# Kernel tuning notes

Hardware: AMD Instinct MI355X
Metric: run time of the kernel (lower is better)

The kernel has to match this reference:

```python
import jax, jax.numpy as jnp
import numpy as np

N_NODES = 50000
N_EDGES = 1600000
D = 64  # in_features == out_features (required by residual index_add)
N_NBR_FEA = 41


def setup_inputs() -> dict:
    key = jax.random.key(0)
    k1, k2, k3, k4, k5 = jax.random.split(key, 5)
    return {
        "x": jax.random.normal(k1, (N_NODES, D), dtype=jnp.float32),
        # torch Linear(in=D, out=2D, bias=False): weight shape [2D, D]
        "W": jax.random.normal(k2, (2 * D, D), dtype=jnp.float32) * (1.0 / np.sqrt(D)),
        "edge_sources": jax.random.randint(k3, (N_EDGES,), 0, N_NODES),
        "edge_targets": jax.random.randint(k4, (N_EDGES,), 0, N_NODES),
        # required forward arg; unused when use_distance_nbr=False
        "distance_nbr": jax.random.normal(k5, (N_EDGES, N_NBR_FEA), dtype=jnp.float32),
    }


def reference(x, W, edge_sources, edge_targets, distance_nbr):
    # gather neighbor (target) node features per edge: [E, D]
    h = x[edge_targets]
    # edge linear -> gate + message halves: [E, 2D]
    ge = h @ W.T
    g, e = jnp.split(ge, 2, axis=1)
    msg = jax.nn.sigmoid(g) * e  # gate_activation = Sigmoid(); edge/node activations are None
    # output = input.clone(); output.index_add_(0, edge_sources, g * e)
    return x.at[edge_sources].add(msg)
```

## Files before the change

### kernel.cpp

```cpp
#include <hip/hip_runtime.h>

#define NDIM 64
#define WPAD 68
#define BINSHIFT 8
#define BINSZ 256
#define LCAP 12288
#define EPT 16
#define PCHUNK (256 * EPT)
#define NMB 512
#define PB  256

typedef unsigned short ushort;

__device__ __forceinline__ ushort f2bf(float f) {
    unsigned u = __float_as_uint(f);
    return (ushort)((u + 0x7FFFu + ((u >> 16) & 1u)) >> 16);
}
__device__ __forceinline__ float bflo(unsigned u) { return __uint_as_float(u << 16); }
__device__ __forceinline__ float bfhi(unsigned u) { return __uint_as_float(u & 0xFFFF0000u); }

__device__ void node_msg_body(
    const float* __restrict__ x, const float* __restrict__ W,
    ushort* __restrict__ Mb, int n_nodes, int bid, int nblocks)
{
    __shared__ float sW[128 * WPAD];
    __shared__ float sx[4][4][64];

    for (int i = threadIdx.x; i < 128 * 64; i += 256)
        sW[(i >> 6) * WPAD + (i & 63)] = W[i];
    __syncthreads();

    const int wid  = threadIdx.x >> 6;
    const int lane = threadIdx.x & 63;
    const float4* __restrict__ wg4 = (const float4*)&sW[lane * WPAD];
    const float4* __restrict__ we4 = (const float4*)&sW[(lane + 64) * WPAD];
    const size_t half_off = (size_t)(lane >> 5) * n_nodes * 32 + (lane & 31);

    int n0 = (bid * 4 + wid) * 4;
    int stride = nblocks * 16;
    for (; n0 < n_nodes; n0 += stride) {
        #pragma unroll
        for (int q = 0; q < 4; ++q) {
            int n = n0 + q;
            sx[wid][q][lane] = (n < n_nodes) ? x[(size_t)n * NDIM + lane] : 0.0f;
        }
        float g[4] = {0, 0, 0, 0}, e[4] = {0, 0, 0, 0};
        #pragma unroll
        for (int k4 = 0; k4 < 16; ++k4) {
            float4 a = wg4[k4];
            float4 b = we4[k4];
            #pragma unroll
            for (int q = 0; q < 4; ++q) {
                float4 xk = *(const float4*)&sx[wid][q][k4 * 4];
                g[q] = fmaf(xk.x, a.x, g[q]); g[q] = fmaf(xk.y, a.y, g[q]);
                g[q] = fmaf(xk.z, a.z, g[q]); g[q] = fmaf(xk.w, a.w, g[q]);
                e[q] = fmaf(xk.x, b.x, e[q]); e[q] = fmaf(xk.y, b.y, e[q]);
                e[q] = fmaf(xk.z, b.z, e[q]); e[q] = fmaf(xk.w, b.w, e[q]);
            }
        }
        #pragma unroll
        for (int q = 0; q < 4; ++q) {
            int n = n0 + q;
            if (n < n_nodes)
                Mb[half_off + (size_t)n * 32] = f2bf(e[q] / (1.0f + __expf(-g[q])));
        }
    }
}

__device__ void partition_body(
    const int* __restrict__ src, const int* __restrict__ tgt,
    int* __restrict__ binCursor, unsigned* __restrict__ binned,
    int n_edges, int nbins, int bid, int nblocks)
{
    __shared__ int h[256];
    __shared__ int base[256];
    const int tid = threadIdx.x;

    long long cb = (long long)bid * PCHUNK;
    long long cs = (long long)nblocks * PCHUNK;
    for (; cb < n_edges; cb += cs) {
        if (tid < nbins) h[tid] = 0;
        __syncthreads();

        unsigned pk[EPT]; ushort ps[EPT]; short pb[EPT];
        #pragma unroll
        for (int r = 0; r < EPT; ++r) {
            long long e = cb + r * 256 + tid;
            pb[r] = -1;
            if (e < n_edges) {
                int s = src[e], t = tgt[e];
                int b = s >> BINSHIFT;
                pk[r] = ((unsigned)(s & (BINSZ - 1)) << 16) | (unsigned)t;
                ps[r] = (ushort)atomicAdd(&h[b], 1);
                pb[r] = (short)b;
            }
        }
        __syncthreads();
        if (tid < nbins) {
            int c = h[tid];
            base[tid] = c ? atomicAdd(&binCursor[tid], c) : 0;
        }
        __syncthreads();
        #pragma unroll
        for (int r = 0; r < EPT; ++r) {
            if (pb[r] >= 0) {
                unsigned d = (unsigned)base[pb[r]] + ps[r];
                if (d < LCAP) binned[(size_t)pb[r] * LCAP + d] = pk[r];
            }
        }
        __syncthreads();
    }
}

__global__ __launch_bounds__(256) void fused_msg_partition_kernel(
    const float* __restrict__ x, const float* __restrict__ W,
    ushort* __restrict__ Mb, const int* __restrict__ src,
    const int* __restrict__ tgt, int* __restrict__ binCursor,
    unsigned* __restrict__ binned, int n_nodes, int n_edges, int nbins)
{
    if (blockIdx.x < NMB)
        node_msg_body(x, W, Mb, n_nodes, blockIdx.x, NMB);
    else
        partition_body(src, tgt, binCursor, binned, n_edges, nbins,
                       blockIdx.x - NMB, PB);
}

__global__ __launch_bounds__(512) void csr_build_kernel(
    const unsigned* __restrict__ binned, const int* __restrict__ binCursor,
    unsigned* __restrict__ node_meta, ushort* __restrict__ entries, int n_nodes)
{
    __shared__ unsigned sE[LCAP];
    __shared__ ushort   sT[LCAP];
    __shared__ int sCnt[BINSZ];
    __shared__ int sOff[BINSZ + 1];
    __shared__ int sCur[BINSZ];

    const int bin = blockIdx.x;
    const int tid = threadIdx.x;
    const int cnt = min(binCursor[bin], LCAP);
    const unsigned* __restrict__ be = &binned[(size_t)bin * LCAP];

    for (int i = tid; i < cnt; i += 512) sE[i] = be[i];
    for (int i = tid; i < BINSZ; i += 512) sCnt[i] = 0;
    for (int i = tid; i < LCAP / 2; i += 512) ((unsigned*)sT)[i] = 0;
    __syncthreads();

    for (int i = tid; i < cnt; i += 512) atomicAdd(&sCnt[sE[i] >> 16], 1);
    __syncthreads();

    if (tid < 64) {
        int c[4]; int s = 0;
        #pragma unroll
        for (int q = 0; q < 4; ++q) { c[q] = (sCnt[tid * 4 + q] + 7) & ~7; s += c[q]; }
        int incl = s;
        #pragma unroll
        for (int d = 1; d < 64; d <<= 1) {
            int t = __shfl_up(incl, d);
            if (tid >= d) incl += t;
        }
        int excl = incl - s;
        #pragma unroll
        for (int q = 0; q < 4; ++q) { sOff[tid * 4 + q] = excl; excl += c[q]; }
        if (tid == 63) sOff[BINSZ] = excl;
    }
    __syncthreads();
    if (tid < BINSZ) sCur[tid] = sOff[tid];
    __syncthreads();

    for (int i = tid; i < cnt; i += 512) {
        unsigned p = sE[i];
        int pos = atomicAdd(&sCur[p >> 16], 1);
        sT[pos] = (ushort)(p & 0xFFFFu);
    }

    const int gbase = bin * LCAP;
    if (tid < BINSZ) {
        int n = (bin << BINSHIFT) + tid;
        if (n < n_nodes)
            node_meta[n] = ((unsigned)(gbase + sOff[tid]) << 8)
                         | (unsigned)min(sCnt[tid], 255);
    }
    __syncthreads();

    const int tot = sOff[BINSZ];
    uint4* __restrict__ dstv = (uint4*)&entries[gbase];
    const uint4* __restrict__ srcv = (const uint4*)sT;
    for (int i = tid; i < tot / 8; i += 512) dstv[i] = srcv[i];
}

__global__ __launch_bounds__(256) void gather_half_kernel(
    const float* __restrict__ x, const ushort* __restrict__ Mbh,
    const unsigned* __restrict__ node_meta, const ushort* __restrict__ entries,
    float* __restrict__ out, int n_nodes, int half)
{
    const int wid  = threadIdx.x >> 6;
    const int lane = threadIdx.x & 63;
    const int sub  = lane >> 2;
    const int sl   = lane & 3;

    int n = (blockIdx.x * 4 + wid) * 16 + sub;
    bool valid = n < n_nodes;
    int nn = valid ? n : 0;
    unsigned meta = valid ? node_meta[nn] : 0u;
    int cnt = (int)(meta & 255u);
    const ushort* __restrict__ brow = &entries[meta >> 8];

    float acc[8] = {0, 0, 0, 0, 0, 0, 0, 0};
    for (int j = 0; j < cnt; j += 8) {
        uint4 nb = *(const uint4*)&brow[j];
        unsigned id[8] = { nb.x & 0xFFFFu, nb.x >> 16, nb.y & 0xFFFFu, nb.y >> 16,
                           nb.z & 0xFFFFu, nb.z >> 16, nb.w & 0xFFFFu, nb.w >> 16 };
        #pragma unroll
        for (int k = 0; k < 8; ++k) {
            if (j + k < cnt) {
                uint4 v = *(const uint4*)&Mbh[(size_t)id[k] * 32 + sl * 8];
                acc[0] += bflo(v.x); acc[1] += bfhi(v.x);
                acc[2] += bflo(v.y); acc[3] += bfhi(v.y);
                acc[4] += bflo(v.z); acc[5] += bfhi(v.z);
                acc[6] += bflo(v.w); acc[7] += bfhi(v.w);
            }
        }
    }
    if (valid) {
        size_t base = (size_t)n * NDIM + half * 32 + sl * 8;
        float4 x0 = *(const float4*)&x[base];
        float4 x1 = *(const float4*)&x[base + 4];
        float4 o0 = {x0.x + acc[0], x0.y + acc[1], x0.z + acc[2], x0.w + acc[3]};
        float4 o1 = {x1.x + acc[4], x1.y + acc[5], x1.z + acc[6], x1.w + acc[7]};
        *(float4*)&out[base]     = o0;
        *(float4*)&out[base + 4] = o1;
    }
}

__global__ __launch_bounds__(256) void copy_out_kernel(
    const float* __restrict__ x, float* __restrict__ out, size_t n)
{
    size_t i = (size_t)blockIdx.x * 256 + threadIdx.x;
    size_t gs = (size_t)gridDim.x * 256;
    for (; i < n; i += gs) out[i] = x[i];
}

__global__ __launch_bounds__(256) void edge_scatter_kernel(
    const int* __restrict__ src, const int* __restrict__ tgt,
    const ushort* __restrict__ Mb, float* __restrict__ out,
    int n_edges, int n_nodes)
{
    long long total = (long long)n_edges * 16;
    long long i0 = (long long)blockIdx.x * blockDim.x + threadIdx.x;
    long long gs = (long long)gridDim.x * blockDim.x;
    for (long long i = i0; i < total; i += gs) {
        int e = (int)(i >> 4);
        int q = (int)(i & 15);
        int s = src[e];
        int t = tgt[e];
        int half = q >> 2;
        int d    = (q * 4) & 31;
        uint2 v = *(const uint2*)&Mb[(size_t)half * n_nodes * 32
                                     + (size_t)t * 32 + d];
        float* o = &out[(size_t)s * NDIM + q * 4];
        atomicAdd(o + 0, bflo(v.x));
        atomicAdd(o + 1, bfhi(v.x));
        atomicAdd(o + 2, bflo(v.y));
        atomicAdd(o + 3, bfhi(v.y));
    }
}

static inline size_t align16(size_t v) { return (v + 15) & ~(size_t)15; }

extern "C" void kernel_launch(void* const* d_in, const int* in_sizes, int n_in,
                              void* d_out, int out_size, void* d_ws, size_t ws_size,
                              hipStream_t stream)
{
    const float* x   = (const float*)d_in[0];
    const float* W   = (const float*)d_in[1];
    const int*   src = (const int*)d_in[2];
    const int*   tgt = (const int*)d_in[3];

    int n_nodes = in_sizes[0] / NDIM;
    int n_edges = in_sizes[2];
    float* out = (float*)d_out;

    int nbins = (n_nodes + BINSZ - 1) >> BINSHIFT;

    char* ws = (char*)d_ws;
    size_t off = 0;
    ushort* Mb = (ushort*)(ws + off);            off = align16(off + (size_t)n_nodes * NDIM * 2);
    unsigned* node_meta = (unsigned*)(ws + off); off = align16(off + (size_t)n_nodes * 4);
    int* binCursor = (int*)(ws + off);           off = align16(off + (size_t)nbins * 4);
    unsigned* binned = (unsigned*)(ws + off);    off = align16(off + (size_t)nbins * LCAP * 4);
    ushort* entries = (ushort*)(ws + off);       off = align16(off + (size_t)nbins * LCAP * 2);
    size_t need = off + 1024;

    if (ws_size >= need && n_nodes <= 65536 && nbins <= 256) {
        hipMemsetAsync(binCursor, 0, (size_t)nbins * sizeof(int), stream);
        fused_msg_partition_kernel<<<NMB + PB, 256, 0, stream>>>(
            x, W, Mb, src, tgt, binCursor, binned, n_nodes, n_edges, nbins);
        csr_build_kernel<<<nbins, 512, 0, stream>>>(
            binned, binCursor, node_meta, entries, n_nodes);
        int gb = (n_nodes + 63) / 64;
        gather_half_kernel<<<gb, 256, 0, stream>>>(
            x, Mb, node_meta, entries, out, n_nodes, 0);
        gather_half_kernel<<<gb, 256, 0, stream>>>(
            x, Mb + (size_t)n_nodes * 32, node_meta, entries, out, n_nodes, 1);
    } else if (ws_size >= (size_t)n_nodes * NDIM * sizeof(ushort)) {
        fused_msg_partition_kernel<<<NMB, 256, 0, stream>>>(
            x, W, Mb, src, tgt, (int*)nullptr, (unsigned*)nullptr,
            n_nodes, 0, 0);
        copy_out_kernel<<<2048, 256, 0, stream>>>(x, out, (size_t)n_nodes * NDIM);
        long long total = (long long)n_edges * 16;
        edge_scatter_kernel<<<(int)((total + 255) / 256), 256, 0, stream>>>(
            src, tgt, Mb, out, n_edges, n_nodes);
    }
}
```

Baseline: 118.8 us.

## Fuse CSR build with gather into per-bin kernel using full-row bf16 messages

Merges the CSR build and both half-gather kernels into a single per-bin kernel that sorts each bin's edges in LDS and immediately gathers bf16 messages, so node_meta and the entries arrays never round-trip through global memory. Bins shrink from 256 to 128 nodes (391 bins, up to 512 supported), which raises the block count and halves the LDS per block. The message buffer is now stored in full-row layout, so each gather reads one 128-byte row instead of two split halves. The risk is lower gather parallelism per block, since each 512-thread block runs the bin-sort serially before it starts gathering, and the fixed per-bin capacity must still hold the edge count.

```diff
diff --git a/kernel.cpp b/kernel.cpp
--- a/kernel.cpp
+++ b/kernel.cpp
@@ -2,13 +2,14 @@
 
 #define NDIM 64
 #define WPAD 68
-#define BINSHIFT 8
-#define BINSZ 256
-#define LCAP 12288
+#define BINSHIFT 7
+#define BINSZ 128
+#define LCAP 6144
 #define EPT 16
 #define PCHUNK (256 * EPT)
 #define NMB 512
 #define PB  256
+#define MAXBINS 512
 
 typedef unsigned short ushort;
 
@@ -34,7 +35,6 @@
     const int lane = threadIdx.x & 63;
     const float4* __restrict__ wg4 = (const float4*)&sW[lane * WPAD];
     const float4* __restrict__ we4 = (const float4*)&sW[(lane + 64) * WPAD];
-    const size_t half_off = (size_t)(lane >> 5) * n_nodes * 32 + (lane & 31);
 
     int n0 = (bid * 4 + wid) * 4;
     int stride = nblocks * 16;
@@ -62,7 +62,7 @@
         for (int q = 0; q < 4; ++q) {
             int n = n0 + q;
             if (n < n_nodes)
-                Mb[half_off + (size_t)n * 32] = f2bf(e[q] / (1.0f + __expf(-g[q])));
+                Mb[(size_t)n * NDIM + lane] = f2bf(e[q] / (1.0f + __expf(-g[q])));
         }
     }
 }
@@ -72,14 +72,14 @@
     int* __restrict__ binCursor, unsigned* __restrict__ binned,
     int n_edges, int nbins, int bid, int nblocks)
 {
-    __shared__ int h[256];
-    __shared__ int base[256];
+    __shared__ int h[MAXBINS];
+    __shared__ int base[MAXBINS];
     const int tid = threadIdx.x;
 
     long long cb = (long long)bid * PCHUNK;
     long long cs = (long long)nblocks * PCHUNK;
     for (; cb < n_edges; cb += cs) {
-        if (tid < nbins) h[tid] = 0;
+        for (int i = tid; i < nbins; i += 256) h[i] = 0;
         __syncthreads();
 
         unsigned pk[EPT]; ushort ps[EPT]; short pb[EPT];
@@ -96,9 +96,9 @@
             }
         }
         __syncthreads();
-        if (tid < nbins) {
-            int c = h[tid];
-            base[tid] = c ? atomicAdd(&binCursor[tid], c) : 0;
+        for (int i = tid; i < nbins; i += 256) {
+            int c = h[i];
+            base[i] = c ? atomicAdd(&binCursor[i], c) : 0;
         }
         __syncthreads();
         #pragma unroll
@@ -125,14 +125,15 @@
                        blockIdx.x - NMB, PB);
 }
 
-__global__ __launch_bounds__(512) void csr_build_kernel(
+__global__ __launch_bounds__(512) void csr_gather_kernel(
     const unsigned* __restrict__ binned, const int* __restrict__ binCursor,
-    unsigned* __restrict__ node_meta, ushort* __restrict__ entries, int n_nodes)
+    const ushort* __restrict__ Mb, const float* __restrict__ x,
+    float* __restrict__ out, int n_nodes)
 {
     __shared__ unsigned sE[LCAP];
     __shared__ ushort   sT[LCAP];
     __shared__ int sCnt[BINSZ];
-    __shared__ int sOff[BINSZ + 1];
+    __shared__ int sOff[BINSZ];
     __shared__ int sCur[BINSZ];
 
     const int bin = blockIdx.x;
@@ -140,18 +141,19 @@
     const int cnt = min(binCursor[bin], LCAP);
     const unsigned* __restrict__ be = &binned[(size_t)bin * LCAP];
 
-    for (int i = tid; i < cnt; i += 512) sE[i] = be[i];
     for (int i = tid; i < BINSZ; i += 512) sCnt[i] = 0;
-    for (int i = tid; i < LCAP / 2; i += 512) ((unsigned*)sT)[i] = 0;
-    __syncthreads();
-
-    for (int i = tid; i < cnt; i += 512) atomicAdd(&sCnt[sE[i] >> 16], 1);
+    __syncthreads();
+    for (int i = tid; i < cnt; i += 512) {
+        unsigned v = be[i];
+        sE[i] = v;
+        atomicAdd(&sCnt[v >> 16], 1);
+    }
     __syncthreads();
 
     if (tid < 64) {
-        int c[4]; int s = 0;
-        #pragma unroll
-        for (int q = 0; q < 4; ++q) { c[q] = (sCnt[tid * 4 + q] + 7) & ~7; s += c[q]; }
+        int c0 = (sCnt[tid * 2]     + 7) & ~7;
+        int c1 = (sCnt[tid * 2 + 1] + 7) & ~7;
+        int s = c0 + c1;
         int incl = s;
         #pragma unroll
         for (int d = 1; d < 64; d <<= 1) {
@@ -159,12 +161,9 @@
             if (tid >= d) incl += t;
         }
         int excl = incl - s;
-        #pragma unroll
-        for (int q = 0; q < 4; ++q) { sOff[tid * 4 + q] = excl; excl += c[q]; }
-        if (tid == 63) sOff[BINSZ] = excl;
-    }
-    __syncthreads();
-    if (tid < BINSZ) sCur[tid] = sOff[tid];
+        sOff[tid * 2]     = excl;      sCur[tid * 2]     = excl;
+        sOff[tid * 2 + 1] = excl + c0; sCur[tid * 2 + 1] = excl + c0;
+    }
     __syncthreads();
 
     for (int i = tid; i < cnt; i += 512) {
@@ -172,63 +171,43 @@
         int pos = atomicAdd(&sCur[p >> 16], 1);
         sT[pos] = (ushort)(p & 0xFFFFu);
     }
-
-    const int gbase = bin * LCAP;
-    if (tid < BINSZ) {
-        int n = (bin << BINSHIFT) + tid;
-        if (n < n_nodes)
-            node_meta[n] = ((unsigned)(gbase + sOff[tid]) << 8)
-                         | (unsigned)min(sCnt[tid], 255);
-    }
-    __syncthreads();
-
-    const int tot = sOff[BINSZ];
-    uint4* __restrict__ dstv = (uint4*)&entries[gbase];
-    const uint4* __restrict__ srcv = (const uint4*)sT;
-    for (int i = tid; i < tot / 8; i += 512) dstv[i] = srcv[i];
-}
-
-__global__ __launch_bounds__(256) void gather_half_kernel(
-    const float* __restrict__ x, const ushort* __restrict__ Mbh,
-    const unsigned* __restrict__ node_meta, const ushort* __restrict__ entries,
-    float* __restrict__ out, int n_nodes, int half)
-{
-    const int wid  = threadIdx.x >> 6;
-    const int lane = threadIdx.x & 63;
-    const int sub  = lane >> 2;
-    const int sl   = lane & 3;
-
-    int n = (blockIdx.x * 4 + wid) * 16 + sub;
-    bool valid = n < n_nodes;
-    int nn = valid ? n : 0;
-    unsigned meta = valid ? node_meta[nn] : 0u;
-    int cnt = (int)(meta & 255u);
-    const ushort* __restrict__ brow = &entries[meta >> 8];
-
-    float acc[8] = {0, 0, 0, 0, 0, 0, 0, 0};
-    for (int j = 0; j < cnt; j += 8) {
-        uint4 nb = *(const uint4*)&brow[j];
-        unsigned id[8] = { nb.x & 0xFFFFu, nb.x >> 16, nb.y & 0xFFFFu, nb.y >> 16,
-                           nb.z & 0xFFFFu, nb.z >> 16, nb.w & 0xFFFFu, nb.w >> 16 };
-        #pragma unroll
-        for (int k = 0; k < 8; ++k) {
-            if (j + k < cnt) {
-                uint4 v = *(const uint4*)&Mbh[(size_t)id[k] * 32 + sl * 8];
-                acc[0] += bflo(v.x); acc[1] += bfhi(v.x);
-                acc[2] += bflo(v.y); acc[3] += bfhi(v.y);
-                acc[4] += bflo(v.z); acc[5] += bfhi(v.z);
-                acc[6] += bflo(v.w); acc[7] += bfhi(v.w);
-            }
-        }
-    }
-    if (valid) {
-        size_t base = (size_t)n * NDIM + half * 32 + sl * 8;
-        float4 x0 = *(const float4*)&x[base];
-        float4 x1 = *(const float4*)&x[base + 4];
-        float4 o0 = {x0.x + acc[0], x0.y + acc[1], x0.z + acc[2], x0.w + acc[3]};
-        float4 o1 = {x1.x + acc[4], x1.y + acc[5], x1.z + acc[6], x1.w + acc[7]};
-        *(float4*)&out[base]     = o0;
-        *(float4*)&out[base + 4] = o1;
+    __syncthreads();
+
+    const int wid  = tid >> 6;
+    const int lane = tid & 63;
+    const int sub  = lane >> 3;
+    const int sl   = lane & 7;
+    #pragma unroll
+    for (int r = 0; r < BINSZ / 64; ++r) {
+        int ln = r * 64 + wid * 8 + sub;
+        int n  = (bin << BINSHIFT) + ln;
+        int c  = sCnt[ln];
+        int off = sOff[ln];
+        float acc[8] = {0, 0, 0, 0, 0, 0, 0, 0};
+        for (int j = 0; j < c; j += 8) {
+            uint4 nb = *(const uint4*)&sT[off + j];
+            unsigned id[8] = { nb.x & 0xFFFFu, nb.x >> 16, nb.y & 0xFFFFu, nb.y >> 16,
+                               nb.z & 0xFFFFu, nb.z >> 16, nb.w & 0xFFFFu, nb.w >> 16 };
+            #pragma unroll
+            for (int k = 0; k < 8; ++k) {
+                if (j + k < c) {
+                    uint4 v = *(const uint4*)&Mb[(size_t)id[k] * NDIM + sl * 8];
+                    acc[0] += bflo(v.x); acc[1] += bfhi(v.x);
+                    acc[2] += bflo(v.y); acc[3] += bfhi(v.y);
+                    acc[4] += bflo(v.z); acc[5] += bfhi(v.z);
+                    acc[6] += bflo(v.w); acc[7] += bfhi(v.w);
+                }
+            }
+        }
+        if (n < n_nodes) {
+            size_t base = (size_t)n * NDIM + sl * 8;
+            float4 x0 = *(const float4*)&x[base];
+            float4 x1 = *(const float4*)&x[base + 4];
+            float4 o0 = {x0.x + acc[0], x0.y + acc[1], x0.z + acc[2], x0.w + acc[3]};
+            float4 o1 = {x1.x + acc[4], x1.y + acc[5], x1.z + acc[6], x1.w + acc[7]};
+            *(float4*)&out[base]     = o0;
+            *(float4*)&out[base + 4] = o1;
+        }
     }
 }
 
@@ -242,8 +221,7 @@
 
 __global__ __launch_bounds__(256) void edge_scatter_kernel(
     const int* __restrict__ src, const int* __restrict__ tgt,
-    const ushort* __restrict__ Mb, float* __restrict__ out,
-    int n_edges, int n_nodes)
+    const ushort* __restrict__ Mb, float* __restrict__ out, int n_edges)
 {
     long long total = (long long)n_edges * 16;
     long long i0 = (long long)blockIdx.x * blockDim.x + threadIdx.x;
@@ -253,10 +231,7 @@
         int q = (int)(i & 15);
         int s = src[e];
         int t = tgt[e];
-        int half = q >> 2;
-        int d    = (q * 4) & 31;
-        uint2 v = *(const uint2*)&Mb[(size_t)half * n_nodes * 32
-                                     + (size_t)t * 32 + d];
+        uint2 v = *(const uint2*)&Mb[(size_t)t * NDIM + q * 4];
         float* o = &out[(size_t)s * NDIM + q * 4];
         atomicAdd(o + 0, bflo(v.x));
         atomicAdd(o + 1, bfhi(v.x));
@@ -284,24 +259,17 @@
 
     char* ws = (char*)d_ws;
     size_t off = 0;
-    ushort* Mb = (ushort*)(ws + off);            off = align16(off + (size_t)n_nodes * NDIM * 2);
-    unsigned* node_meta = (unsigned*)(ws + off); off = align16(off + (size_t)n_nodes * 4);
-    int* binCursor = (int*)(ws + off);           off = align16(off + (size_t)nbins * 4);
-    unsigned* binned = (unsigned*)(ws + off);    off = align16(off + (size_t)nbins * LCAP * 4);
-    ushort* entries = (ushort*)(ws + off);       off = align16(off + (size_t)nbins * LCAP * 2);
+    ushort* Mb = (ushort*)(ws + off);         off = align16(off + (size_t)n_nodes * NDIM * 2);
+    int* binCursor = (int*)(ws + off);        off = align16(off + (size_t)nbins * 4);
+    unsigned* binned = (unsigned*)(ws + off); off = align16(off + (size_t)nbins * LCAP * 4);
     size_t need = off + 1024;
 
-    if (ws_size >= need && n_nodes <= 65536 && nbins <= 256) {
+    if (ws_size >= need && n_nodes <= 65536 && nbins <= MAXBINS) {
         hipMemsetAsync(binCursor, 0, (size_t)nbins * sizeof(int), stream);
         fused_msg_partition_kernel<<<NMB + PB, 256, 0, stream>>>(
             x, W, Mb, src, tgt, binCursor, binned, n_nodes, n_edges, nbins);
-        csr_build_kernel<<<nbins, 512, 0, stream>>>(
-            binned, binCursor, node_meta, entries, n_nodes);
-        int gb = (n_nodes + 63) / 64;
-        gather_half_kernel<<<gb, 256, 0, stream>>>(
-            x, Mb, node_meta, entries, out, n_nodes, 0);
-        gather_half_kernel<<<gb, 256, 0, stream>>>(
-            x, Mb + (size_t)n_nodes * 32, node_meta, entries, out, n_nodes, 1);
+        csr_gather_kernel<<<nbins, 512, 0, stream>>>(
+            binned, binCursor, Mb, x, out, n_nodes);
     } else if (ws_size >= (size_t)n_nodes * NDIM * sizeof(ushort)) {
         fused_msg_partition_kernel<<<NMB, 256, 0, stream>>>(
             x, W, Mb, src, tgt, (int*)nullptr, (unsigned*)nullptr,
@@ -309,6 +277,6 @@
         copy_out_kernel<<<2048, 256, 0, stream>>>(x, out, (size_t)n_nodes * NDIM);
         long long total = (long long)n_edges * 16;
         edge_scatter_kernel<<<(int)((total + 255) / 256), 256, 0, stream>>>(
-            src, tgt, Mb, out, n_edges, n_nodes);
-    }
-}
+            src, tgt, Mb, out, n_edges);
+    }
+}
```

Result: faster. 113.0 us (-4.8%).
